# Optimization experiments

Hardware: AMD Instinct MI355X
Metric: run time of the kernel (lower is better)

## Reference

```python
import jax, jax.numpy as jnp
import numpy as np

B, D, L = 32, 512, 4096   # batch, latent_dim (dim1), time length
N, D2 = 77, 768           # text tokens, text_latent_dim (dim2)
BC = 24                   # number of conditioned batch elements
H = 8                     # num_heads
EPS = 1e-5


def _layernorm(x, g, b):
    mu = jnp.mean(x, axis=-1, keepdims=True)
    var = jnp.mean(jnp.square(x - mu), axis=-1, keepdims=True)
    return (x - mu) * jax.lax.rsqrt(var + EPS) * g + b


def setup_inputs() -> dict:
    key = jax.random.key(0)
    ks = jax.random.split(key, 8)
    s = 0.02
    return {
        "input_tensor": jax.random.normal(ks[0], (B, D, L), jnp.float32),
        "condition_tensor": jax.random.normal(ks[1], (B, N, D2), jnp.float32),
        "cond_indices": jnp.arange(BC, dtype=jnp.int64 if jax.config.jax_enable_x64 else jnp.int32),
        "ln_g": jnp.ones((D,), jnp.float32),
        "ln_b": jnp.zeros((D,), jnp.float32),
        "tln_g": jnp.ones((D2,), jnp.float32),
        "tln_b": jnp.zeros((D2,), jnp.float32),
        "Wq": jax.random.normal(ks[2], (D, D), jnp.float32) * s,
        "bq": jnp.zeros((D,), jnp.float32),
        "Wk": jax.random.normal(ks[3], (D2, D), jnp.float32) * s,
        "bk": jnp.zeros((D,), jnp.float32),
        "Wv": jax.random.normal(ks[4], (D2, D), jnp.float32) * s,
        "bv": jnp.zeros((D,), jnp.float32),
    }


def reference(input_tensor, condition_tensor, cond_indices,
              ln_g, ln_b, tln_g, tln_b, Wq, bq, Wk, bk, Wv, bv):
    dh = D // H
    # gather conditioned rows; [Bc, D, L] -> [Bc, T=L, D]
    x_cond = jnp.transpose(input_tensor[cond_indices], (0, 2, 1))
    cond = condition_tensor[cond_indices]  # [Bc, N, D2]

    q = _layernorm(x_cond, ln_g, ln_b) @ Wq + bq           # [Bc, T, D]
    cn = _layernorm(cond, tln_g, tln_b)                     # [Bc, N, D2]
    k = (cn @ Wk + bk).reshape(BC, N, H, dh)
    v = (cn @ Wv + bv).reshape(BC, N, H, dh)

    q = jax.nn.softmax(q.reshape(BC, L, H, dh), axis=-1)   # feature-map softmax
    k = jax.nn.softmax(k, axis=1)                           # softmax over tokens N

    context = jnp.einsum('bnhk,bnhv->bhkv', k, v)           # [Bc, H, dh, dh]
    y = jnp.einsum('bthk,bhkv->bthv', q, context).reshape(BC, L, D)

    # scatter residual back: indices are unique, so .add == torch index assignment
    return input_tensor.at[cond_indices].add(jnp.transpose(y, (0, 2, 1)))
```

## Files before the change

kernel.cpp:

```cpp
#include <hip/hip_runtime.h>
#include <hip/hip_bf16.h>

#define LN_EPS 1e-5f

typedef __attribute__((ext_vector_type(8))) short bf16x8;
typedef __attribute__((ext_vector_type(4))) float f32x4;

__device__ __forceinline__ unsigned short f2bf(float f){
  unsigned u = __builtin_bit_cast(unsigned, f);
  u = (u + 0x7fffu + ((u >> 16) & 1u)) >> 16;
  return (unsigned short)u;
}
__device__ __forceinline__ float bf2f(unsigned short h){
  unsigned u = ((unsigned)h) << 16;
  return __builtin_bit_cast(float, u);
}
__device__ __forceinline__ void gll16(const void* g, void* l){
  __builtin_amdgcn_global_load_lds(
      (const __attribute__((address_space(1))) unsigned int*)(g),
      (__attribute__((address_space(3))) unsigned int*)(l), 16, 0, 0);
}

__global__ void k_prep(const float* __restrict__ Wq, const float* __restrict__ ln_g,
                       const float* __restrict__ ln_b,
                       unsigned short* __restrict__ gWqT, float2* __restrict__ c12)
{
  __shared__ float r1[64][4], r2[64][4];
  const int tid = threadIdx.x;
  const int n0 = blockIdx.x * 64;
  const int c = tid & 63, q = tid >> 6;
  float c1p = 0.f, c2p = 0.f;
  for(int i=0;i<128;i+=4){
    ushort4 pk;
    unsigned short* pp = (unsigned short*)&pk;
    #pragma unroll
    for(int j=0;j<4;j++){
      const int d = q*128 + i + j;
      const float wv = Wq[(size_t)d*512 + n0 + c];
      const float gw = ln_g[d] * wv;
      const unsigned short hb = f2bf(gw);
      pp[j] = hb;
      c2p += bf2f(hb);
      c1p += ln_b[d] * wv;
    }
    *(ushort4*)(gWqT + (size_t)(n0 + c)*512 + q*128 + i) = pk;
  }
  r1[c][q] = c1p; r2[c][q] = c2p;
  __syncthreads();
  if(q == 0){
    float a = 0.f, b2 = 0.f;
    #pragma unroll
    for(int j=0;j<4;j++){ a += r1[c][j]; b2 += r2[c][j]; }
    c12[n0 + c] = make_float2(a, b2);
  }
}

__global__ void k_condkv(const float* __restrict__ cond, const int* __restrict__ idx,
                         const float* __restrict__ tg, const float* __restrict__ tb,
                         const float* __restrict__ Wk, const float* __restrict__ bk,
                         const float* __restrict__ Wv, const float* __restrict__ bv,
                         float* __restrict__ kbuf, float* __restrict__ vbuf)
{
  __shared__ float cn[16][768];
  const int bc = blockIdx.z, nc = blockIdx.y, dc = blockIdx.x;
  const int b = idx[bc];
  const int n0 = nc * 16;
  int nrows = 77 - n0; if(nrows > 16) nrows = 16;
  const int w = threadIdx.x >> 6, lane = threadIdx.x & 63;

  for(int r = w; r < nrows; r += 4){
    const float* src = cond + ((size_t)b * 77 + n0 + r) * 768;
    float vals[12]; float s1 = 0.f, s2 = 0.f;
    #pragma unroll
    for(int i=0;i<12;i++){ float x = src[lane + i*64]; vals[i]=x; s1+=x; s2+=x*x; }
    #pragma unroll
    for(int off=1; off<64; off<<=1){ s1 += __shfl_xor(s1, off); s2 += __shfl_xor(s2, off); }
    const float mu  = s1 * (1.f/768.f);
    const float var = s2 * (1.f/768.f) - mu*mu;
    const float rs  = rsqrtf(var + LN_EPS);
    #pragma unroll
    for(int i=0;i<12;i++){ const int c2 = lane + i*64; cn[r][c2] = (vals[i]-mu)*rs*tg[c2] + tb[c2]; }
  }
  __syncthreads();

  const int dq = threadIdx.x & 63;
  const int part = threadIdx.x >> 6;
  const float* W    = (dc < 2) ? Wk : Wv;
  const float* bias = (dc < 2) ? bk : bv;
  float* obuf       = (dc < 2) ? kbuf : vbuf;
  const int d0 = (dc & 1) * 256 + dq * 4;

  float acc[4][4] = {};
  for(int i=0;i<768;i++){
    const float4 wv = *(const float4*)(W + (size_t)i * 512 + d0);
    #pragma unroll
    for(int j=0;j<4;j++){
      const float c = cn[part*4 + j][i];
      acc[j][0] += c * wv.x; acc[j][1] += c * wv.y;
      acc[j][2] += c * wv.z; acc[j][3] += c * wv.w;
    }
  }
  #pragma unroll
  for(int j=0;j<4;j++){
    const int r = part*4 + j, n = n0 + r;
    if(r < nrows){
      float4 o;
      o.x = acc[j][0] + bias[d0+0];
      o.y = acc[j][1] + bias[d0+1];
      o.z = acc[j][2] + bias[d0+2];
      o.w = acc[j][3] + bias[d0+3];
      *(float4*)(obuf + ((size_t)bc * 77 + n) * 512 + d0) = o;
    }
  }
}

__global__ void k_ctx(const float* __restrict__ kbuf, const float* __restrict__ vbuf,
                      unsigned short* __restrict__ ctxP)
{
  __shared__ float kk[77][64];
  __shared__ float vv[77][64];
  __shared__ float inv_s[64];
  const int h = blockIdx.x, bc = blockIdx.y;
  const int tid = threadIdx.x;
  for(int e = tid; e < 77*64; e += 256){
    const int n = e >> 6, c = e & 63;
    kk[n][c] = kbuf[((size_t)bc * 77 + n) * 512 + h*64 + c];
    vv[n][c] = vbuf[((size_t)bc * 77 + n) * 512 + h*64 + c];
  }
  __syncthreads();
  if(tid < 64){
    float m = -1e30f;
    for(int n=0;n<77;n++) m = fmaxf(m, kk[n][tid]);
    float s = 0.f;
    for(int n=0;n<77;n++){ const float e = __expf(kk[n][tid] - m); kk[n][tid] = e; s += e; }
    inv_s[tid] = 1.f / s;
  }
  __syncthreads();
  #pragma unroll
  for(int j=0;j<16;j++){
    const int o = tid + 256*j;
    const int v = o >> 6, k2 = o & 63;
    float a = 0.f;
    for(int n=0;n<77;n++) a += kk[n][k2] * vv[n][v];
    const int pos = ((((k2>>5)*4 + (v>>4))*4 + ((k2>>3)&3))*16 + (v&15))*8 + (k2&7);
    ctxP[((size_t)(bc*8 + h)) * 4096 + pos] = f2bf(a * inv_s[k2]);
  }
}

__global__ void k_copy(const float* __restrict__ in, const int* __restrict__ idx,
                       float* __restrict__ out)
{
  const int b = blockIdx.y;
  bool member = false;
  for(int i=0;i<24;i++) member |= (idx[i] == b);
  if(member) return;
  const float4* s = (const float4*)(in  + (size_t)b * 512 * 4096);
  float4*       d = (float4*)      (out + (size_t)b * 512 * 4096);
  for(int i = blockIdx.x*256 + threadIdx.x; i < 512*4096/4; i += 128*256) d[i] = s[i];
}

__global__ __launch_bounds__(256, 3)
void k_gemm2(const float* __restrict__ input, const int* __restrict__ idx,
             const unsigned short* __restrict__ gWqT, const float2* __restrict__ c12,
             const float* __restrict__ bq, const unsigned short* __restrict__ ctxP,
             float* __restrict__ out)
{
  __shared__ __align__(16) char smem[49152];
  float*          Xs0 = (float*)(smem);
  unsigned short* Ws0 = (unsigned short*)(smem + 16384);
  float*          Xs1 = (float*)(smem + 24576);
  unsigned short* Ws1 = (unsigned short*)(smem + 40960);
  unsigned short* P   = (unsigned short*)(smem);
  float*          red = (float*)(smem + 36864);
  float*          mu_s= (float*)(smem + 38912);
  float*          rs_s= (float*)(smem + 39424);

  const int tid  = threadIdx.x;
  const int lane = tid & 63;
  const int w    = tid >> 6;
  const int col  = lane & 15;
  const int g    = lane >> 4;
  const int wm   = w >> 1, wn = w & 1;
  const int ntile = blockIdx.x, mtile = blockIdx.y;
  const int bc   = mtile >> 5;
  const int tt0  = (mtile & 31) * 128;
  const int b    = idx[bc];
  const int nbase = ntile * 128;
  const char* xbase = (const char*)(input + (size_t)b * 512 * 4096) + (size_t)tt0 * 4;
  const char* wbase = (const char*)gWqT + (size_t)nbase * 1024;

  const int tstat = tid & 127;
  const int hstat = tid >> 7;
  float s1 = 0.f, s2 = 0.f;

  float* Xbuf[2] = {Xs0, Xs1};
  unsigned short* Wbuf[2] = {Ws0, Ws1};

  #define STAGE(ks, bi)                                                          \
  {                                                                              \
    _Pragma("unroll")                                                            \
    for(int i=0;i<4;i++){                                                        \
      const int f = tid*16 + i*4096;                                             \
      const int kk_ = f >> 9, oo_ = f & 511;                                     \
      gll16(xbase + (size_t)((ks)*32 + kk_) * 16384 + oo_, (char*)Xbuf[bi] + f); \
    }                                                                            \
    _Pragma("unroll")                                                            \
    for(int i=0;i<2;i++){                                                        \
      const int f = tid*16 + i*4096;                                             \
      const int nn_ = f >> 6, oo_ = f & 63;                                      \
      gll16(wbase + (size_t)nn_ * 1024 + (ks)*64 + oo_, (char*)Wbuf[bi] + f);    \
    }                                                                            \
  }

  f32x4 acc[4][4] = {};

  STAGE(0, 0);
  __syncthreads();

  for(int ks=0; ks<16; ++ks){
    const int cur = ks & 1;
    if(ks < 15) STAGE(ks+1, cur^1);

    const float* X = Xbuf[cur];
    const unsigned short* W = Wbuf[cur];

    bf16x8 af[4];
    #pragma unroll
    for(int mt=0; mt<4; ++mt){
      const int t = wm*64 + mt*16 + col;
      union { unsigned short s[8]; bf16x8 v; } u;
      #pragma unroll
      for(int j=0;j<8;++j){
        const float fv = X[(g*8 + j)*128 + t];
        u.s[j] = __bfloat16_as_ushort(__float2bfloat16(fv));
      }
      af[mt] = u.v;
    }
    bf16x8 bfr[4];
    #pragma unroll
    for(int nt=0; nt<4; ++nt)
      bfr[nt] = *(const bf16x8*)(W + (size_t)(wn*64 + nt*16 + col)*32 + g*8);

    #pragma unroll
    for(int mt=0; mt<4; ++mt)
      #pragma unroll
      for(int nt=0; nt<4; ++nt)
        acc[mt][nt] = __builtin_amdgcn_mfma_f32_16x16x32_bf16(af[mt], bfr[nt], acc[mt][nt], 0, 0, 0);

    #pragma unroll
    for(int i=0;i<16;++i){
      const float xv = X[(hstat*16 + i)*128 + tstat];
      s1 += xv; s2 += xv*xv;
    }
    __syncthreads();
  }
  #undef STAGE

  red[tstat*4 + hstat*2 + 0] = s1;
  red[tstat*4 + hstat*2 + 1] = s2;
  __syncthreads();
  if(tid < 128){
    const float a = red[tid*4 + 0] + red[tid*4 + 2];
    const float c = red[tid*4 + 1] + red[tid*4 + 3];
    const float mu = a * (1.f/512.f);
    const float var = c * (1.f/512.f) - mu*mu;
    mu_s[tid] = mu;
    rs_s[tid] = rsqrtf(var + LN_EPS);
  }
  __syncthreads();

  float c1b[4], c2v[4];
  #pragma unroll
  for(int nt=0; nt<4; ++nt){
    const int n = nbase + wn*64 + nt*16 + col;
    const float2 cc = c12[n];
    c1b[nt] = cc.x + bq[n];
    c2v[nt] = cc.y;
  }
  #pragma unroll
  for(int mt=0; mt<4; ++mt){
    #pragma unroll
    for(int r=0; r<4; ++r){
      const int t = wm*64 + mt*16 + g*4 + r;
      const float mur = mu_s[t], rsr = rs_s[t];
      const float mrc = rsr * mur;
      float v[4];
      #pragma unroll
      for(int nt=0; nt<4; ++nt)
        v[nt] = rsr*acc[mt][nt][r] - mrc*c2v[nt] + c1b[nt];
      float m = fmaxf(fmaxf(v[0],v[1]), fmaxf(v[2],v[3]));
      m = fmaxf(m, __shfl_xor(m, 1));
      m = fmaxf(m, __shfl_xor(m, 2));
      m = fmaxf(m, __shfl_xor(m, 4));
      m = fmaxf(m, __shfl_xor(m, 8));
      float s = 0.f;
      #pragma unroll
      for(int nt=0; nt<4; ++nt){ v[nt] = __expf(v[nt] - m); s += v[nt]; }
      s += __shfl_xor(s, 1);
      s += __shfl_xor(s, 2);
      s += __shfl_xor(s, 4);
      s += __shfl_xor(s, 8);
      const float inv = 1.f / s;
      #pragma unroll
      for(int nt=0; nt<4; ++nt) acc[mt][nt][r] = v[nt] * inv;
    }
  }

  unsigned short* Pw = P + w * 64 * 72;
  #pragma unroll
  for(int mt=0; mt<4; ++mt)
    #pragma unroll
    for(int nt=0; nt<4; ++nt)
      #pragma unroll
      for(int r=0; r<4; ++r)
        Pw[(mt*16 + g*4 + r)*72 + nt*16 + col] = f2bf(acc[mt][nt][r]);

  const int head = ntile*2 + wn;
  const unsigned short* cp = ctxP + (size_t)(bc*8 + head) * 4096;
  f32x4 y[4][4] = {};
  #pragma unroll
  for(int ks2=0; ks2<2; ++ks2){
    bf16x8 pa[4];
    #pragma unroll
    for(int mt=0; mt<4; ++mt)
      pa[mt] = *(const bf16x8*)(Pw + (mt*16 + col)*72 + ks2*32 + g*8);
    bf16x8 cv[4];
    #pragma unroll
    for(int vt=0; vt<4; ++vt)
      cv[vt] = *(const bf16x8*)(cp + (size_t)(((ks2*4 + vt)*4 + g)*16 + col) * 8);
    #pragma unroll
    for(int mt=0; mt<4; ++mt)
      #pragma unroll
      for(int vt=0; vt<4; ++vt)
        y[mt][vt] = __builtin_amdgcn_mfma_f32_16x16x32_bf16(pa[mt], cv[vt], y[mt][vt], 0, 0, 0);
  }

  const float* xb = input + (size_t)b * 512 * 4096;
  float*       ob = out   + (size_t)b * 512 * 4096;
  #pragma unroll
  for(int mt=0; mt<4; ++mt)
    #pragma unroll
    for(int vt=0; vt<4; ++vt){
      const size_t row = (size_t)(head*64 + vt*16 + col);
      const size_t a = row*4096 + (size_t)(tt0 + wm*64 + mt*16 + g*4);
      const float4 xr = *(const float4*)(xb + a);
      float4 o4;
      o4.x = xr.x + y[mt][vt][0];
      o4.y = xr.y + y[mt][vt][1];
      o4.z = xr.z + y[mt][vt][2];
      o4.w = xr.w + y[mt][vt][3];
      *(float4*)(ob + a) = o4;
    }
}

extern "C" void kernel_launch(void* const* d_in, const int* in_sizes, int n_in,
                              void* d_out, int out_size, void* d_ws, size_t ws_size,
                              hipStream_t stream)
{
  const float* input = (const float*)d_in[0];
  const float* cond  = (const float*)d_in[1];
  const int*   idx   = (const int*)d_in[2];
  const float* ln_g  = (const float*)d_in[3];
  const float* ln_b  = (const float*)d_in[4];
  const float* tln_g = (const float*)d_in[5];
  const float* tln_b = (const float*)d_in[6];
  const float* Wq    = (const float*)d_in[7];
  const float* bq    = (const float*)d_in[8];
  const float* Wk    = (const float*)d_in[9];
  const float* bk    = (const float*)d_in[10];
  const float* Wv    = (const float*)d_in[11];
  const float* bv    = (const float*)d_in[12];
  float* out = (float*)d_out;
  char*  ws  = (char*)d_ws;

  unsigned short* gWqT = (unsigned short*)(ws);
  float2*         c12  = (float2*)(ws + 524288);
  unsigned short* ctxP = (unsigned short*)(ws + 528384);
  float* kbuf = (float*)(ws + 2101248);
  float* vbuf = (float*)(ws + 2101248 + 3784704);

  k_prep  <<<dim3(8),       dim3(256), 0, stream>>>(Wq, ln_g, ln_b, gWqT, c12);
  k_condkv<<<dim3(4,5,24),  dim3(256), 0, stream>>>(cond, idx, tln_g, tln_b, Wk, bk, Wv, bv, kbuf, vbuf);
  k_ctx   <<<dim3(8,24),    dim3(256), 0, stream>>>(kbuf, vbuf, ctxP);
  k_copy  <<<dim3(128,32),  dim3(256), 0, stream>>>(input, idx, out);
  k_gemm2 <<<dim3(4,768),   dim3(256), 0, stream>>>(input, idx, gWqT, c12, bq, ctxP, out);
}
```

Measured before the change: 449.8 us.

## Split LayerNorm into separate transpose kernel feeding bf16 swizzled GEMM

Adds a kernel that gathers the conditioned rows, applies LayerNorm and writes a transposed, XOR-swizzled bf16 copy of activations. The Q GEMM then streams bf16 tiles for both operands directly, with no in-loop fp32-to-bf16 conversion, no statistics accumulation and no folded-LN correction terms. This gives a smaller shared-memory footprint and higher occupancy. The cost is an extra round trip through global memory for a roughly 100 MB bf16 intermediate, plus one more kernel launch.

```diff
diff --git a/kernel.cpp b/kernel.cpp
--- a/kernel.cpp
+++ b/kernel.cpp
@@ -4,6 +4,7 @@
 #define LN_EPS 1e-5f
 
 typedef __attribute__((ext_vector_type(8))) short bf16x8;
+typedef __attribute__((ext_vector_type(8))) short s16x8;
 typedef __attribute__((ext_vector_type(4))) float f32x4;
 
 __device__ __forceinline__ unsigned short f2bf(float f){
@@ -11,48 +12,17 @@
   u = (u + 0x7fffu + ((u >> 16) & 1u)) >> 16;
   return (unsigned short)u;
 }
-__device__ __forceinline__ float bf2f(unsigned short h){
-  unsigned u = ((unsigned)h) << 16;
-  return __builtin_bit_cast(float, u);
-}
 __device__ __forceinline__ void gll16(const void* g, void* l){
   __builtin_amdgcn_global_load_lds(
       (const __attribute__((address_space(1))) unsigned int*)(g),
       (__attribute__((address_space(3))) unsigned int*)(l), 16, 0, 0);
 }
 
-__global__ void k_prep(const float* __restrict__ Wq, const float* __restrict__ ln_g,
-                       const float* __restrict__ ln_b,
-                       unsigned short* __restrict__ gWqT, float2* __restrict__ c12)
-{
-  __shared__ float r1[64][4], r2[64][4];
-  const int tid = threadIdx.x;
-  const int n0 = blockIdx.x * 64;
-  const int c = tid & 63, q = tid >> 6;
-  float c1p = 0.f, c2p = 0.f;
-  for(int i=0;i<128;i+=4){
-    ushort4 pk;
-    unsigned short* pp = (unsigned short*)&pk;
-    #pragma unroll
-    for(int j=0;j<4;j++){
-      const int d = q*128 + i + j;
-      const float wv = Wq[(size_t)d*512 + n0 + c];
-      const float gw = ln_g[d] * wv;
-      const unsigned short hb = f2bf(gw);
-      pp[j] = hb;
-      c2p += bf2f(hb);
-      c1p += ln_b[d] * wv;
-    }
-    *(ushort4*)(gWqT + (size_t)(n0 + c)*512 + q*128 + i) = pk;
-  }
-  r1[c][q] = c1p; r2[c][q] = c2p;
-  __syncthreads();
-  if(q == 0){
-    float a = 0.f, b2 = 0.f;
-    #pragma unroll
-    for(int j=0;j<4;j++){ a += r1[c][j]; b2 += r2[c][j]; }
-    c12[n0 + c] = make_float2(a, b2);
-  }
+__global__ void k_wqt(const float* __restrict__ Wq, unsigned short* __restrict__ WqT){
+  const int tid = blockIdx.x * 256 + threadIdx.x;
+  const int d = tid >> 9, n = tid & 511;
+  const int swz = (n >> 1) & 3;
+  WqT[(size_t)n * 512 + (d ^ (swz << 3))] = f2bf(Wq[(size_t)d * 512 + n]);
 }
 
 __global__ void k_condkv(const float* __restrict__ cond, const int* __restrict__ idx,
@@ -159,21 +129,99 @@
   for(int i = blockIdx.x*256 + threadIdx.x; i < 512*4096/4; i += 128*256) d[i] = s[i];
 }
 
-__global__ __launch_bounds__(256, 3)
-void k_gemm2(const float* __restrict__ input, const int* __restrict__ idx,
-             const unsigned short* __restrict__ gWqT, const float2* __restrict__ c12,
+__global__ __launch_bounds__(256, 2)
+void k_lnt(const float* __restrict__ input, const int* __restrict__ idx,
+           const float* __restrict__ ln_g, const float* __restrict__ ln_b,
+           unsigned short* __restrict__ xT)
+{
+  __shared__ float buf[32][516];
+  __shared__ float red1[32][8], red2[32][8];
+  __shared__ float mu_s[32], rs_s[32];
+  __shared__ float gbuf[512], bbuf[512];
+
+  const int tid = threadIdx.x;
+  const int bc = blockIdx.y;
+  const int b  = idx[bc];
+  const int t0 = blockIdx.x * 32;
+  const float* xb = input + (size_t)b * (512*4096) + t0;
+
+  *(float2*)&gbuf[tid*2] = *(const float2*)&ln_g[tid*2];
+  *(float2*)&bbuf[tid*2] = *(const float2*)&ln_b[tid*2];
+
+  {
+    const int p  = tid & 7;
+    const int dg = tid >> 3;
+    #pragma unroll
+    for(int i=0;i<16;i++){
+      const int d = dg + i*32;
+      const float4 x = *(const float4*)(xb + (size_t)d * 4096 + p*4);
+      buf[p*4+0][d] = x.x; buf[p*4+1][d] = x.y;
+      buf[p*4+2][d] = x.z; buf[p*4+3][d] = x.w;
+    }
+  }
+  __syncthreads();
+
+  {
+    const int t = tid & 31, part = tid >> 5;
+    float s1 = 0.f, s2 = 0.f;
+    #pragma unroll
+    for(int i=0;i<16;i++){
+      const float4 v = *(const float4*)&buf[t][part*64 + i*4];
+      s1 += v.x+v.y+v.z+v.w;
+      s2 += v.x*v.x + v.y*v.y + v.z*v.z + v.w*v.w;
+    }
+    red1[t][part] = s1; red2[t][part] = s2;
+  }
+  __syncthreads();
+  if(tid < 32){
+    float a = 0.f, c = 0.f;
+    #pragma unroll
+    for(int p=0;p<8;p++){ a += red1[tid][p]; c += red2[tid][p]; }
+    const float mu  = a * (1.f/512.f);
+    const float var = c * (1.f/512.f) - mu*mu;
+    mu_s[tid] = mu; rs_s[tid] = rsqrtf(var + LN_EPS);
+  }
+  __syncthreads();
+
+  {
+    const int c  = tid & 7;
+    const int tt = tid >> 3;
+    const float mu = mu_s[tt], rs = rs_s[tt];
+    const int swz = (tt >> 1) & 3;
+    unsigned short* orow = xT + ((size_t)bc*4096 + t0 + tt) * 512;
+    #pragma unroll
+    for(int j=0;j<8;j++){
+      const int d0 = c*8 + j*64;
+      const float4 a  = *(const float4*)&buf[tt][d0];
+      const float4 b4 = *(const float4*)&buf[tt][d0+4];
+      const float4 g0 = *(const float4*)&gbuf[d0];
+      const float4 g1 = *(const float4*)&gbuf[d0+4];
+      const float4 h0 = *(const float4*)&bbuf[d0];
+      const float4 h1 = *(const float4*)&bbuf[d0+4];
+      s16x8 o;
+      o[0] = (short)f2bf((a.x -mu)*rs*g0.x + h0.x);
+      o[1] = (short)f2bf((a.y -mu)*rs*g0.y + h0.y);
+      o[2] = (short)f2bf((a.z -mu)*rs*g0.z + h0.z);
+      o[3] = (short)f2bf((a.w -mu)*rs*g0.w + h0.w);
+      o[4] = (short)f2bf((b4.x-mu)*rs*g1.x + h1.x);
+      o[5] = (short)f2bf((b4.y-mu)*rs*g1.y + h1.y);
+      o[6] = (short)f2bf((b4.z-mu)*rs*g1.z + h1.z);
+      o[7] = (short)f2bf((b4.w-mu)*rs*g1.w + h1.w);
+      *(s16x8*)(orow + (d0 ^ (swz << 3))) = o;
+    }
+  }
+}
+
+__global__ __launch_bounds__(256, 4)
+void k_gemm3(const float* __restrict__ input, const int* __restrict__ idx,
+             const unsigned short* __restrict__ xT, const unsigned short* __restrict__ WqT,
              const float* __restrict__ bq, const unsigned short* __restrict__ ctxP,
              float* __restrict__ out)
 {
-  __shared__ __align__(16) char smem[49152];
-  float*          Xs0 = (float*)(smem);
-  unsigned short* Ws0 = (unsigned short*)(smem + 16384);
-  float*          Xs1 = (float*)(smem + 24576);
-  unsigned short* Ws1 = (unsigned short*)(smem + 40960);
-  unsigned short* P   = (unsigned short*)(smem);
-  float*          red = (float*)(smem + 36864);
-  float*          mu_s= (float*)(smem + 38912);
-  float*          rs_s= (float*)(smem + 39424);
+  __shared__ __align__(16) char smem[36864];
+  char* Ab[2] = { smem,         smem + 16384 };
+  char* Bb[2] = { smem + 8192,  smem + 24576 };
+  unsigned short* P = (unsigned short*)smem;
 
   const int tid  = threadIdx.x;
   const int lane = tid & 63;
@@ -186,123 +234,85 @@
   const int tt0  = (mtile & 31) * 128;
   const int b    = idx[bc];
   const int nbase = ntile * 128;
-  const char* xbase = (const char*)(input + (size_t)b * 512 * 4096) + (size_t)tt0 * 4;
-  const char* wbase = (const char*)gWqT + (size_t)nbase * 1024;
-
-  const int tstat = tid & 127;
-  const int hstat = tid >> 7;
-  float s1 = 0.f, s2 = 0.f;
-
-  float* Xbuf[2] = {Xs0, Xs1};
-  unsigned short* Wbuf[2] = {Ws0, Ws1};
-
-  #define STAGE(ks, bi)                                                          \
-  {                                                                              \
-    _Pragma("unroll")                                                            \
-    for(int i=0;i<4;i++){                                                        \
-      const int f = tid*16 + i*4096;                                             \
-      const int kk_ = f >> 9, oo_ = f & 511;                                     \
-      gll16(xbase + (size_t)((ks)*32 + kk_) * 16384 + oo_, (char*)Xbuf[bi] + f); \
-    }                                                                            \
-    _Pragma("unroll")                                                            \
-    for(int i=0;i<2;i++){                                                        \
-      const int f = tid*16 + i*4096;                                             \
-      const int nn_ = f >> 6, oo_ = f & 63;                                      \
-      gll16(wbase + (size_t)nn_ * 1024 + (ks)*64 + oo_, (char*)Wbuf[bi] + f);    \
-    }                                                                            \
+  const char* xTb = (const char*)xT + ((size_t)bc*4096 + tt0) * 1024;
+  const char* wTb = (const char*)WqT + (size_t)nbase * 1024;
+
+  const int f0 = tid * 16;
+  const int f1 = f0 + 4096;
+  const int r0 = f0 >> 6, o0 = f0 & 63;
+  const int r1 = f1 >> 6, o1 = f1 & 63;
+
+  #define STAGE(ks, bi)                                          \
+  {                                                              \
+    gll16(xTb + (size_t)r0*1024 + (ks)*64 + o0, Ab[bi] + f0);    \
+    gll16(xTb + (size_t)r1*1024 + (ks)*64 + o1, Ab[bi] + f1);    \
+    gll16(wTb + (size_t)r0*1024 + (ks)*64 + o0, Bb[bi] + f0);    \
+    gll16(wTb + (size_t)r1*1024 + (ks)*64 + o1, Bb[bi] + f1);    \
   }
 
   f32x4 acc[4][4] = {};
 
+  int offA[4], offB[4];
+  #pragma unroll
+  for(int mt=0; mt<4; ++mt){
+    const int rowA = wm*64 + mt*16 + col;
+    offA[mt] = rowA*64 + ((g ^ ((rowA>>1)&3)) << 4);
+    const int rowB = wn*64 + mt*16 + col;
+    offB[mt] = rowB*64 + ((g ^ ((rowB>>1)&3)) << 4);
+  }
+
   STAGE(0, 0);
-  __syncthreads();
+  asm volatile("s_waitcnt vmcnt(0)" ::: "memory");
+  __builtin_amdgcn_s_barrier();
 
   for(int ks=0; ks<16; ++ks){
     const int cur = ks & 1;
     if(ks < 15) STAGE(ks+1, cur^1);
 
-    const float* X = Xbuf[cur];
-    const unsigned short* W = Wbuf[cur];
-
-    bf16x8 af[4];
-    #pragma unroll
-    for(int mt=0; mt<4; ++mt){
-      const int t = wm*64 + mt*16 + col;
-      union { unsigned short s[8]; bf16x8 v; } u;
-      #pragma unroll
-      for(int j=0;j<8;++j){
-        const float fv = X[(g*8 + j)*128 + t];
-        u.s[j] = __bfloat16_as_ushort(__float2bfloat16(fv));
-      }
-      af[mt] = u.v;
-    }
-    bf16x8 bfr[4];
-    #pragma unroll
-    for(int nt=0; nt<4; ++nt)
-      bfr[nt] = *(const bf16x8*)(W + (size_t)(wn*64 + nt*16 + col)*32 + g*8);
-
+    bf16x8 af[4], bfr[4];
+    #pragma unroll
+    for(int mt=0; mt<4; ++mt) af[mt]  = *(const bf16x8*)(Ab[cur] + offA[mt]);
+    #pragma unroll
+    for(int nt=0; nt<4; ++nt) bfr[nt] = *(const bf16x8*)(Bb[cur] + offB[nt]);
     #pragma unroll
     for(int mt=0; mt<4; ++mt)
       #pragma unroll
       for(int nt=0; nt<4; ++nt)
         acc[mt][nt] = __builtin_amdgcn_mfma_f32_16x16x32_bf16(af[mt], bfr[nt], acc[mt][nt], 0, 0, 0);
 
-    #pragma unroll
-    for(int i=0;i<16;++i){
-      const float xv = X[(hstat*16 + i)*128 + tstat];
-      s1 += xv; s2 += xv*xv;
-    }
-    __syncthreads();
+    asm volatile("s_waitcnt vmcnt(0)" ::: "memory");
+    __builtin_amdgcn_s_barrier();
   }
   #undef STAGE
 
-  red[tstat*4 + hstat*2 + 0] = s1;
-  red[tstat*4 + hstat*2 + 1] = s2;
-  __syncthreads();
-  if(tid < 128){
-    const float a = red[tid*4 + 0] + red[tid*4 + 2];
-    const float c = red[tid*4 + 1] + red[tid*4 + 3];
-    const float mu = a * (1.f/512.f);
-    const float var = c * (1.f/512.f) - mu*mu;
-    mu_s[tid] = mu;
-    rs_s[tid] = rsqrtf(var + LN_EPS);
-  }
-  __syncthreads();
-
-  float c1b[4], c2v[4];
-  #pragma unroll
-  for(int nt=0; nt<4; ++nt){
-    const int n = nbase + wn*64 + nt*16 + col;
-    const float2 cc = c12[n];
-    c1b[nt] = cc.x + bq[n];
-    c2v[nt] = cc.y;
-  }
   #pragma unroll
   for(int mt=0; mt<4; ++mt){
     #pragma unroll
-    for(int r=0; r<4; ++r){
-      const int t = wm*64 + mt*16 + g*4 + r;
-      const float mur = mu_s[t], rsr = rs_s[t];
-      const float mrc = rsr * mur;
-      float v[4];
-      #pragma unroll
-      for(int nt=0; nt<4; ++nt)
-        v[nt] = rsr*acc[mt][nt][r] - mrc*c2v[nt] + c1b[nt];
-      float m = fmaxf(fmaxf(v[0],v[1]), fmaxf(v[2],v[3]));
+    for(int nt=0; nt<4; ++nt){
+      const float bqv = bq[nbase + wn*64 + nt*16 + col];
+      #pragma unroll
+      for(int r=0;r<4;++r) acc[mt][nt][r] += bqv;
+    }
+    #pragma unroll
+    for(int r=0;r<4;++r){
+      float m = fmaxf(fmaxf(acc[mt][0][r],acc[mt][1][r]), fmaxf(acc[mt][2][r],acc[mt][3][r]));
       m = fmaxf(m, __shfl_xor(m, 1));
       m = fmaxf(m, __shfl_xor(m, 2));
       m = fmaxf(m, __shfl_xor(m, 4));
       m = fmaxf(m, __shfl_xor(m, 8));
       float s = 0.f;
       #pragma unroll
-      for(int nt=0; nt<4; ++nt){ v[nt] = __expf(v[nt] - m); s += v[nt]; }
+      for(int q=0;q<4;++q){
+        const float e = __expf(acc[mt][q][r] - m);
+        acc[mt][q][r] = e; s += e;
+      }
       s += __shfl_xor(s, 1);
       s += __shfl_xor(s, 2);
       s += __shfl_xor(s, 4);
       s += __shfl_xor(s, 8);
       const float inv = 1.f / s;
       #pragma unroll
-      for(int nt=0; nt<4; ++nt) acc[mt][nt][r] = v[nt] * inv;
+      for(int q=0;q<4;++q) acc[mt][q][r] *= inv;
     }
   }
 
@@ -373,15 +383,16 @@
   float* out = (float*)d_out;
   char*  ws  = (char*)d_ws;
 
-  unsigned short* gWqT = (unsigned short*)(ws);
-  float2*         c12  = (float2*)(ws + 524288);
-  unsigned short* ctxP = (unsigned short*)(ws + 528384);
-  float* kbuf = (float*)(ws + 2101248);
-  float* vbuf = (float*)(ws + 2101248 + 3784704);
-
-  k_prep  <<<dim3(8),       dim3(256), 0, stream>>>(Wq, ln_g, ln_b, gWqT, c12);
+  unsigned short* WqT  = (unsigned short*)(ws);
+  unsigned short* ctxP = (unsigned short*)(ws + 524288);
+  float* kbuf = (float*)(ws + 2097152);
+  float* vbuf = (float*)(ws + 2097152 + 3784704);
+  unsigned short* xT = (unsigned short*)(ws + 2097152 + 2*3784704);
+
+  k_wqt   <<<dim3(1024),    dim3(256), 0, stream>>>(Wq, WqT);
   k_condkv<<<dim3(4,5,24),  dim3(256), 0, stream>>>(cond, idx, tln_g, tln_b, Wk, bk, Wv, bv, kbuf, vbuf);
   k_ctx   <<<dim3(8,24),    dim3(256), 0, stream>>>(kbuf, vbuf, ctxP);
   k_copy  <<<dim3(128,32),  dim3(256), 0, stream>>>(input, idx, out);
-  k_gemm2 <<<dim3(4,768),   dim3(256), 0, stream>>>(input, idx, gWqT, c12, bq, ctxP, out);
-}
+  k_lnt   <<<dim3(128,24),  dim3(256), 0, stream>>>(input, idx, ln_g, ln_b, xT);
+  k_gemm3 <<<dim3(4,768),   dim3(256), 0, stream>>>(input, idx, xT, WqT, bq, ctxP, out);
+}
```

Result: no change. 446.3 us (-0.8%).

## Fuse passthrough copy into GEMM kernel, widen N tile, stage X as bf16

Applied to the files above, without the earlier changes.

Merges the copy of unconditioned batches into the main GEMM launch as extra blocks, removing one kernel launch and letting the copy overlap the compute. The GEMM tile grows to 256 columns per block (two heads per wave), and X is loaded through registers, converted to bf16 once and stored into XOR-swizzled shared memory, replacing the per-MFMA float-to-bf16 conversion from fp32 LDS. The weight layout is swizzled in prep to match, and bq is folded into c12. The larger accumulator tile raises register pressure and lowers occupancy to two blocks per CU.

```diff
diff --git a/kernel.cpp b/kernel.cpp
--- a/kernel.cpp
+++ b/kernel.cpp
@@ -1,5 +1,4 @@
 #include <hip/hip_runtime.h>
-#include <hip/hip_bf16.h>
 
 #define LN_EPS 1e-5f
 
@@ -22,13 +21,15 @@
 }
 
 __global__ void k_prep(const float* __restrict__ Wq, const float* __restrict__ ln_g,
-                       const float* __restrict__ ln_b,
+                       const float* __restrict__ ln_b, const float* __restrict__ bq,
                        unsigned short* __restrict__ gWqT, float2* __restrict__ c12)
 {
   __shared__ float r1[64][4], r2[64][4];
   const int tid = threadIdx.x;
   const int n0 = blockIdx.x * 64;
   const int c = tid & 63, q = tid >> 6;
+  const int n = n0 + c;
+  const int swz = (n >> 1) & 3;
   float c1p = 0.f, c2p = 0.f;
   for(int i=0;i<128;i+=4){
     ushort4 pk;
@@ -36,14 +37,13 @@
     #pragma unroll
     for(int j=0;j<4;j++){
       const int d = q*128 + i + j;
-      const float wv = Wq[(size_t)d*512 + n0 + c];
-      const float gw = ln_g[d] * wv;
-      const unsigned short hb = f2bf(gw);
+      const float wv = Wq[(size_t)d*512 + n];
+      const unsigned short hb = f2bf(ln_g[d] * wv);
       pp[j] = hb;
       c2p += bf2f(hb);
       c1p += ln_b[d] * wv;
     }
-    *(ushort4*)(gWqT + (size_t)(n0 + c)*512 + q*128 + i) = pk;
+    *(ushort4*)(gWqT + (size_t)n*512 + ((q*128 + i) ^ (swz << 3))) = pk;
   }
   r1[c][q] = c1p; r2[c][q] = c2p;
   __syncthreads();
@@ -51,7 +51,7 @@
     float a = 0.f, b2 = 0.f;
     #pragma unroll
     for(int j=0;j<4;j++){ a += r1[c][j]; b2 += r2[c][j]; }
-    c12[n0 + c] = make_float2(a, b2);
+    c12[n] = make_float2(a + bq[n], b2);
   }
 }
 
@@ -147,210 +147,242 @@
   }
 }
 
-__global__ void k_copy(const float* __restrict__ in, const int* __restrict__ idx,
-                       float* __restrict__ out)
+__global__ __launch_bounds__(256, 2)
+void k_fused(const float* __restrict__ input, const int* __restrict__ idx,
+             const unsigned short* __restrict__ gWqT, const float2* __restrict__ c12,
+             const unsigned short* __restrict__ ctxP, float* __restrict__ out)
 {
-  const int b = blockIdx.y;
-  bool member = false;
-  for(int i=0;i<24;i++) member |= (idx[i] == b);
-  if(member) return;
-  const float4* s = (const float4*)(in  + (size_t)b * 512 * 4096);
-  float4*       d = (float4*)      (out + (size_t)b * 512 * 4096);
-  for(int i = blockIdx.x*256 + threadIdx.x; i < 512*4096/4; i += 128*256) d[i] = s[i];
-}
-
-__global__ __launch_bounds__(256, 3)
-void k_gemm2(const float* __restrict__ input, const int* __restrict__ idx,
-             const unsigned short* __restrict__ gWqT, const float2* __restrict__ c12,
-             const float* __restrict__ bq, const unsigned short* __restrict__ ctxP,
-             float* __restrict__ out)
-{
-  __shared__ __align__(16) char smem[49152];
-  float*          Xs0 = (float*)(smem);
-  unsigned short* Ws0 = (unsigned short*)(smem + 16384);
-  float*          Xs1 = (float*)(smem + 24576);
-  unsigned short* Ws1 = (unsigned short*)(smem + 40960);
-  unsigned short* P   = (unsigned short*)(smem);
-  float*          red = (float*)(smem + 36864);
-  float*          mu_s= (float*)(smem + 38912);
-  float*          rs_s= (float*)(smem + 39424);
-
-  const int tid  = threadIdx.x;
-  const int lane = tid & 63;
-  const int w    = tid >> 6;
-  const int col  = lane & 15;
-  const int g    = lane >> 4;
-  const int wm   = w >> 1, wn = w & 1;
-  const int ntile = blockIdx.x, mtile = blockIdx.y;
-  const int bc   = mtile >> 5;
-  const int tt0  = (mtile & 31) * 128;
-  const int b    = idx[bc];
-  const int nbase = ntile * 128;
-  const char* xbase = (const char*)(input + (size_t)b * 512 * 4096) + (size_t)tt0 * 4;
-  const char* wbase = (const char*)gWqT + (size_t)nbase * 1024;
-
-  const int tstat = tid & 127;
-  const int hstat = tid >> 7;
-  float s1 = 0.f, s2 = 0.f;
-
-  float* Xbuf[2] = {Xs0, Xs1};
-  unsigned short* Wbuf[2] = {Ws0, Ws1};
-
-  #define STAGE(ks, bi)                                                          \
-  {                                                                              \
-    _Pragma("unroll")                                                            \
-    for(int i=0;i<4;i++){                                                        \
-      const int f = tid*16 + i*4096;                                             \
-      const int kk_ = f >> 9, oo_ = f & 511;                                     \
-      gll16(xbase + (size_t)((ks)*32 + kk_) * 16384 + oo_, (char*)Xbuf[bi] + f); \
-    }                                                                            \
-    _Pragma("unroll")                                                            \
-    for(int i=0;i<2;i++){                                                        \
-      const int f = tid*16 + i*4096;                                             \
-      const int nn_ = f >> 6, oo_ = f & 63;                                      \
-      gll16(wbase + (size_t)nn_ * 1024 + (ks)*64 + oo_, (char*)Wbuf[bi] + f);    \
-    }                                                                            \
-  }
-
-  f32x4 acc[4][4] = {};
-
-  STAGE(0, 0);
-  __syncthreads();
-
-  for(int ks=0; ks<16; ++ks){
-    const int cur = ks & 1;
-    if(ks < 15) STAGE(ks+1, cur^1);
-
-    const float* X = Xbuf[cur];
-    const unsigned short* W = Wbuf[cur];
-
-    bf16x8 af[4];
-    #pragma unroll
-    for(int mt=0; mt<4; ++mt){
-      const int t = wm*64 + mt*16 + col;
-      union { unsigned short s[8]; bf16x8 v; } u;
-      #pragma unroll
-      for(int j=0;j<8;++j){
-        const float fv = X[(g*8 + j)*128 + t];
-        u.s[j] = __bfloat16_as_ushort(__float2bfloat16(fv));
+  const int ntile = blockIdx.x;
+  const int mtile = blockIdx.y;
+  const int tid = threadIdx.x;
+
+  if(mtile >= 768){
+    const int cid = (mtile - 768)*2 + ntile;
+    const int nb = cid >> 6, chunk = cid & 63;
+    int cnt = 0, bsel = 0;
+    for(int b2 = 0; b2 < 32; ++b2){
+      bool member = false;
+      #pragma unroll
+      for(int i2 = 0; i2 < 24; ++i2) member |= (idx[i2] == b2);
+      if(!member){ if(cnt == nb) bsel = b2; ++cnt; }
+    }
+    const float4* s = (const float4*)(input + (size_t)bsel * 2097152) + chunk*8192;
+    float4*       d = (float4*)      (out   + (size_t)bsel * 2097152) + chunk*8192;
+    #pragma unroll
+    for(int i = 0; i < 32; ++i) d[i*256 + tid] = s[i*256 + tid];
+    return;
+  }
+
+  __shared__ __align__(16) char smem[50176];
+  char* const Xb0 = smem;
+  char* const Wb0 = smem + 8192;
+  char* const Xb1 = smem + 24576;
+  char* const Wb1 = smem + 32768;
+  unsigned short* const P = (unsigned short*)smem;
+  float* const mu_s = (float*)(smem + 49152);
+  float* const rs_s = (float*)(smem + 49664);
+
+  const int lane = tid & 63, w = tid >> 6;
+  const int col = lane & 15, g = lane >> 4;
+  const int wm = w >> 1, wn = w & 1;
+  const int bc = mtile >> 5, b = idx[bc];
+  const int t0 = (mtile & 31) * 128;
+  const int nbase = ntile * 256;
+  const float* xb = input + (size_t)b * 2097152;
+  const char* wTb = (const char*)gWqT + (size_t)nbase * 1024;
+
+  const int tq = tid >> 3;
+  const int kb = tid & 7;
+  const float* xsrc = xb + (size_t)(kb*4) * 4096 + t0 + tq*4;
+
+  int wx[4];
+  #pragma unroll
+  for(int j=0;j<4;j++)
+    wx[j] = (tq*4 + j)*64 + ((((kb>>1) ^ j) & 3) << 4) + ((kb & 1) << 3);
+
+  int offA[4], offB[8];
+  #pragma unroll
+  for(int mt=0; mt<4; ++mt){
+    const int rowA = wm*64 + mt*16 + col;
+    offA[mt] = rowA*64 + ((g ^ (rowA & 3)) << 4);
+  }
+  #pragma unroll
+  for(int nt=0; nt<8; ++nt){
+    const int rowB = wn*128 + nt*16 + col;
+    offB[nt] = rowB*64 + ((g ^ ((rowB >> 1) & 3)) << 4);
+  }
+
+  const int fW = tid * 16;
+
+  #define STAGEW(ks, Wdst)                                                \
+  { _Pragma("unroll")                                                     \
+    for(int i=0;i<4;i++){                                                 \
+      const int f = fW + i*4096;                                          \
+      gll16(wTb + (size_t)(f>>6)*1024 + (ks)*64 + (f&63), (Wdst) + f);    \
+    } }
+  #define LOADX(xr, ks)                                                   \
+  { _Pragma("unroll")                                                     \
+    for(int j=0;j<4;j++) xr[j] = *(const float4*)(xsrc + (size_t)((ks)*32 + j) * 4096); }
+  #define PUTX(xr, Xdst)                                                  \
+  { *(ushort4*)((Xdst) + wx[0]) = make_ushort4(f2bf(xr[0].x), f2bf(xr[1].x), f2bf(xr[2].x), f2bf(xr[3].x)); \
+    *(ushort4*)((Xdst) + wx[1]) = make_ushort4(f2bf(xr[0].y), f2bf(xr[1].y), f2bf(xr[2].y), f2bf(xr[3].y)); \
+    *(ushort4*)((Xdst) + wx[2]) = make_ushort4(f2bf(xr[0].z), f2bf(xr[1].z), f2bf(xr[2].z), f2bf(xr[3].z)); \
+    *(ushort4*)((Xdst) + wx[3]) = make_ushort4(f2bf(xr[0].w), f2bf(xr[1].w), f2bf(xr[2].w), f2bf(xr[3].w)); }
+  #define STATS(xr)                                                       \
+  { s1[0] += xr[0].x + xr[1].x + xr[2].x + xr[3].x;                       \
+    s2[0] += xr[0].x*xr[0].x + xr[1].x*xr[1].x + xr[2].x*xr[2].x + xr[3].x*xr[3].x; \
+    s1[1] += xr[0].y + xr[1].y + xr[2].y + xr[3].y;                       \
+    s2[1] += xr[0].y*xr[0].y + xr[1].y*xr[1].y + xr[2].y*xr[2].y + xr[3].y*xr[3].y; \
+    s1[2] += xr[0].z + xr[1].z + xr[2].z + xr[3].z;                       \
+    s2[2] += xr[0].z*xr[0].z + xr[1].z*xr[1].z + xr[2].z*xr[2].z + xr[3].z*xr[3].z; \
+    s1[3] += xr[0].w + xr[1].w + xr[2].w + xr[3].w;                       \
+    s2[3] += xr[0].w*xr[0].w + xr[1].w*xr[1].w + xr[2].w*xr[2].w + xr[3].w*xr[3].w; }
+
+  f32x4 acc[4][8] = {};
+  float s1[4] = {0,0,0,0}, s2[4] = {0,0,0,0};
+
+  {
+    float4 xr[4];
+    LOADX(xr, 0);
+    STAGEW(0, Wb0);
+    PUTX(xr, Xb0);
+    STATS(xr);
+  }
+  __syncthreads();
+
+  for(int ks = 0; ks < 16; ++ks){
+    char* const Xc = (ks & 1) ? Xb1 : Xb0;
+    char* const Wc = (ks & 1) ? Wb1 : Wb0;
+    char* const Xn = (ks & 1) ? Xb0 : Xb1;
+    char* const Wn = (ks & 1) ? Wb0 : Wb1;
+    float4 xn[4];
+    if(ks < 15){ LOADX(xn, ks+1); STAGEW(ks+1, Wn); }
+
+    bf16x8 af[4], bfr[8];
+    #pragma unroll
+    for(int mt=0; mt<4; ++mt) af[mt]  = *(const bf16x8*)(Xc + offA[mt]);
+    #pragma unroll
+    for(int nt=0; nt<8; ++nt) bfr[nt] = *(const bf16x8*)(Wc + offB[nt]);
+    #pragma unroll
+    for(int mt=0; mt<4; ++mt)
+      #pragma unroll
+      for(int nt=0; nt<8; ++nt)
+        acc[mt][nt] = __builtin_amdgcn_mfma_f32_16x16x32_bf16(af[mt], bfr[nt], acc[mt][nt], 0, 0, 0);
+
+    if(ks < 15){ PUTX(xn, Xn); STATS(xn); }
+    __syncthreads();
+  }
+  #undef STAGEW
+  #undef LOADX
+  #undef PUTX
+  #undef STATS
+
+  #pragma unroll
+  for(int j=0;j<4;j++){
+    #pragma unroll
+    for(int off=1; off<8; off<<=1){
+      s1[j] += __shfl_xor(s1[j], off);
+      s2[j] += __shfl_xor(s2[j], off);
+    }
+  }
+  if(kb == 0){
+    #pragma unroll
+    for(int j=0;j<4;j++){
+      const int t = tq*4 + j;
+      const float mu  = s1[j] * (1.f/512.f);
+      const float var = s2[j] * (1.f/512.f) - mu*mu;
+      mu_s[t] = mu;
+      rs_s[t] = rsqrtf(var + LN_EPS);
+    }
+  }
+  __syncthreads();
+
+  float c1b[8], c2v[8];
+  #pragma unroll
+  for(int nt=0; nt<8; ++nt){
+    const float2 cc = c12[nbase + wn*128 + nt*16 + col];
+    c1b[nt] = cc.x;
+    c2v[nt] = cc.y;
+  }
+  #pragma unroll
+  for(int mt=0; mt<4; ++mt){
+    #pragma unroll
+    for(int r=0; r<4; ++r){
+      const int tl = wm*64 + mt*16 + g*4 + r;
+      const float rsr = rs_s[tl];
+      const float mrc = rsr * mu_s[tl];
+      float v[8];
+      #pragma unroll
+      for(int nt=0; nt<8; ++nt)
+        v[nt] = rsr*acc[mt][nt][r] - mrc*c2v[nt] + c1b[nt];
+      #pragma unroll
+      for(int hh=0; hh<2; ++hh){
+        float m = fmaxf(fmaxf(v[hh*4+0],v[hh*4+1]), fmaxf(v[hh*4+2],v[hh*4+3]));
+        m = fmaxf(m, __shfl_xor(m, 1));
+        m = fmaxf(m, __shfl_xor(m, 2));
+        m = fmaxf(m, __shfl_xor(m, 4));
+        m = fmaxf(m, __shfl_xor(m, 8));
+        float s = 0.f;
+        float e[4];
+        #pragma unroll
+        for(int q2=0;q2<4;++q2){ e[q2] = __expf(v[hh*4+q2] - m); s += e[q2]; }
+        s += __shfl_xor(s, 1);
+        s += __shfl_xor(s, 2);
+        s += __shfl_xor(s, 4);
+        s += __shfl_xor(s, 8);
+        const float inv = 1.f / s;
+        #pragma unroll
+        for(int q2=0;q2<4;++q2) acc[mt][hh*4+q2][r] = e[q2] * inv;
       }
-      af[mt] = u.v;
-    }
-    bf16x8 bfr[4];
-    #pragma unroll
-    for(int nt=0; nt<4; ++nt)
-      bfr[nt] = *(const bf16x8*)(W + (size_t)(wn*64 + nt*16 + col)*32 + g*8);
-
+    }
+  }
+
+  unsigned short* const Pw = P + w * (64*72);
+  float* const ob = out + (size_t)b * 2097152;
+  #pragma unroll
+  for(int hh=0; hh<2; ++hh){
     #pragma unroll
     for(int mt=0; mt<4; ++mt)
       #pragma unroll
-      for(int nt=0; nt<4; ++nt)
-        acc[mt][nt] = __builtin_amdgcn_mfma_f32_16x16x32_bf16(af[mt], bfr[nt], acc[mt][nt], 0, 0, 0);
-
-    #pragma unroll
-    for(int i=0;i<16;++i){
-      const float xv = X[(hstat*16 + i)*128 + tstat];
-      s1 += xv; s2 += xv*xv;
-    }
-    __syncthreads();
-  }
-  #undef STAGE
-
-  red[tstat*4 + hstat*2 + 0] = s1;
-  red[tstat*4 + hstat*2 + 1] = s2;
-  __syncthreads();
-  if(tid < 128){
-    const float a = red[tid*4 + 0] + red[tid*4 + 2];
-    const float c = red[tid*4 + 1] + red[tid*4 + 3];
-    const float mu = a * (1.f/512.f);
-    const float var = c * (1.f/512.f) - mu*mu;
-    mu_s[tid] = mu;
-    rs_s[tid] = rsqrtf(var + LN_EPS);
-  }
-  __syncthreads();
-
-  float c1b[4], c2v[4];
-  #pragma unroll
-  for(int nt=0; nt<4; ++nt){
-    const int n = nbase + wn*64 + nt*16 + col;
-    const float2 cc = c12[n];
-    c1b[nt] = cc.x + bq[n];
-    c2v[nt] = cc.y;
-  }
-  #pragma unroll
-  for(int mt=0; mt<4; ++mt){
-    #pragma unroll
-    for(int r=0; r<4; ++r){
-      const int t = wm*64 + mt*16 + g*4 + r;
-      const float mur = mu_s[t], rsr = rs_s[t];
-      const float mrc = rsr * mur;
-      float v[4];
-      #pragma unroll
-      for(int nt=0; nt<4; ++nt)
-        v[nt] = rsr*acc[mt][nt][r] - mrc*c2v[nt] + c1b[nt];
-      float m = fmaxf(fmaxf(v[0],v[1]), fmaxf(v[2],v[3]));
-      m = fmaxf(m, __shfl_xor(m, 1));
-      m = fmaxf(m, __shfl_xor(m, 2));
-      m = fmaxf(m, __shfl_xor(m, 4));
-      m = fmaxf(m, __shfl_xor(m, 8));
-      float s = 0.f;
-      #pragma unroll
-      for(int nt=0; nt<4; ++nt){ v[nt] = __expf(v[nt] - m); s += v[nt]; }
-      s += __shfl_xor(s, 1);
-      s += __shfl_xor(s, 2);
-      s += __shfl_xor(s, 4);
-      s += __shfl_xor(s, 8);
-      const float inv = 1.f / s;
-      #pragma unroll
-      for(int nt=0; nt<4; ++nt) acc[mt][nt][r] = v[nt] * inv;
-    }
-  }
-
-  unsigned short* Pw = P + w * 64 * 72;
-  #pragma unroll
-  for(int mt=0; mt<4; ++mt)
-    #pragma unroll
-    for(int nt=0; nt<4; ++nt)
-      #pragma unroll
-      for(int r=0; r<4; ++r)
-        Pw[(mt*16 + g*4 + r)*72 + nt*16 + col] = f2bf(acc[mt][nt][r]);
-
-  const int head = ntile*2 + wn;
-  const unsigned short* cp = ctxP + (size_t)(bc*8 + head) * 4096;
-  f32x4 y[4][4] = {};
-  #pragma unroll
-  for(int ks2=0; ks2<2; ++ks2){
-    bf16x8 pa[4];
+      for(int ntl=0; ntl<4; ++ntl)
+        #pragma unroll
+        for(int r=0; r<4; ++r)
+          Pw[(mt*16 + g*4 + r)*72 + ntl*16 + col] = f2bf(acc[mt][hh*4+ntl][r]);
+
+    const int head = ntile*4 + wn*2 + hh;
+    const unsigned short* cp = ctxP + (size_t)(bc*8 + head) * 4096;
+    f32x4 y[4][4] = {};
+    #pragma unroll
+    for(int ks2=0; ks2<2; ++ks2){
+      bf16x8 pa[4];
+      #pragma unroll
+      for(int mt=0; mt<4; ++mt)
+        pa[mt] = *(const bf16x8*)(Pw + (mt*16 + col)*72 + ks2*32 + g*8);
+      bf16x8 cv[4];
+      #pragma unroll
+      for(int vt=0; vt<4; ++vt)
+        cv[vt] = *(const bf16x8*)(cp + (size_t)(((ks2*4 + vt)*4 + g)*16 + col) * 8);
+      #pragma unroll
+      for(int mt=0; mt<4; ++mt)
+        #pragma unroll
+        for(int vt=0; vt<4; ++vt)
+          y[mt][vt] = __builtin_amdgcn_mfma_f32_16x16x32_bf16(pa[mt], cv[vt], y[mt][vt], 0, 0, 0);
+    }
     #pragma unroll
     for(int mt=0; mt<4; ++mt)
-      pa[mt] = *(const bf16x8*)(Pw + (mt*16 + col)*72 + ks2*32 + g*8);
-    bf16x8 cv[4];
-    #pragma unroll
-    for(int vt=0; vt<4; ++vt)
-      cv[vt] = *(const bf16x8*)(cp + (size_t)(((ks2*4 + vt)*4 + g)*16 + col) * 8);
-    #pragma unroll
-    for(int mt=0; mt<4; ++mt)
-      #pragma unroll
-      for(int vt=0; vt<4; ++vt)
-        y[mt][vt] = __builtin_amdgcn_mfma_f32_16x16x32_bf16(pa[mt], cv[vt], y[mt][vt], 0, 0, 0);
-  }
-
-  const float* xb = input + (size_t)b * 512 * 4096;
-  float*       ob = out   + (size_t)b * 512 * 4096;
-  #pragma unroll
-  for(int mt=0; mt<4; ++mt)
-    #pragma unroll
-    for(int vt=0; vt<4; ++vt){
-      const size_t row = (size_t)(head*64 + vt*16 + col);
-      const size_t a = row*4096 + (size_t)(tt0 + wm*64 + mt*16 + g*4);
-      const float4 xr = *(const float4*)(xb + a);
-      float4 o4;
-      o4.x = xr.x + y[mt][vt][0];
-      o4.y = xr.y + y[mt][vt][1];
-      o4.z = xr.z + y[mt][vt][2];
-      o4.w = xr.w + y[mt][vt][3];
-      *(float4*)(ob + a) = o4;
-    }
+      #pragma unroll
+      for(int vt=0; vt<4; ++vt){
+        const size_t a = (size_t)(head*64 + vt*16 + col)*4096
+                       + (size_t)(t0 + wm*64 + mt*16 + g*4);
+        const float4 xr4 = *(const float4*)(xb + a);
+        float4 o4;
+        o4.x = xr4.x + y[mt][vt][0];
+        o4.y = xr4.y + y[mt][vt][1];
+        o4.z = xr4.z + y[mt][vt][2];
+        o4.w = xr4.w + y[mt][vt][3];
+        *(float4*)(ob + a) = o4;
+      }
+  }
 }
 
 extern "C" void kernel_launch(void* const* d_in, const int* in_sizes, int n_in,
@@ -379,9 +411,8 @@
   float* kbuf = (float*)(ws + 2101248);
   float* vbuf = (float*)(ws + 2101248 + 3784704);
 
-  k_prep  <<<dim3(8),       dim3(256), 0, stream>>>(Wq, ln_g, ln_b, gWqT, c12);
+  k_prep  <<<dim3(8),       dim3(256), 0, stream>>>(Wq, ln_g, ln_b, bq, gWqT, c12);
   k_condkv<<<dim3(4,5,24),  dim3(256), 0, stream>>>(cond, idx, tln_g, tln_b, Wk, bk, Wv, bv, kbuf, vbuf);
   k_ctx   <<<dim3(8,24),    dim3(256), 0, stream>>>(kbuf, vbuf, ctxP);
-  k_copy  <<<dim3(128,32),  dim3(256), 0, stream>>>(input, idx, out);
-  k_gemm2 <<<dim3(4,768),   dim3(256), 0, stream>>>(input, idx, gWqT, c12, bq, ctxP, out);
-}
+  k_fused <<<dim3(2,1024),  dim3(256), 0, stream>>>(input, idx, gWqT, c12, ctxP, out);
+}
```

After: 427.6 us. 1.05x faster.
